# Performance work log

Measured on AMD Instinct MI355X. Metric: run time of the kernel, lower is better.

## Reference

```python
import jax, jax.numpy as jnp
import numpy as np

N_HEAD = 4

def setup_inputs() -> dict:
    key = jax.random.key(0)
    ks = jax.random.split(key, 5)
    B, T, C = 2, 4096, 64
    return {
        "x": jax.random.normal(ks[0], (B, T, C), dtype=jnp.float32),
        "w_attn": jax.random.normal(ks[1], (3 * C, C), dtype=jnp.float32) * 0.02,
        "b_attn": jax.random.normal(ks[2], (3 * C,), dtype=jnp.float32) * 0.02,
        "w_proj": jax.random.normal(ks[3], (C, C), dtype=jnp.float32) * 0.02,
        "b_proj": jax.random.normal(ks[4], (C,), dtype=jnp.float32) * 0.02,
    }

def reference(x, w_attn, b_attn, w_proj, b_proj):
    B, T, C = x.shape
    H = N_HEAD
    Dh = C // H
    # fused QKV projection (torch Linear: x @ W.T + b)
    qkv = x @ w_attn.T + b_attn                      # [B,T,3C]
    q, k, v = jnp.split(qkv, 3, axis=-1)             # each [B,T,C]
    q = q.reshape(B, T, H, Dh).transpose(0, 2, 1, 3)  # [B,H,T,Dh]
    k = k.reshape(B, T, H, Dh).transpose(0, 2, 1, 3)
    v = v.reshape(B, T, H, Dh).transpose(0, 2, 1, 3)
    scale = 1.0 / np.sqrt(Dh).astype(np.float32)
    scores = jnp.einsum("bhqd,bhkd->bhqk", q, k) * scale  # [B,H,T,T]
    attn = jax.nn.softmax(scores, axis=-1)
    y = jnp.einsum("bhqk,bhkd->bhqd", attn, v)       # [B,H,T,Dh]
    y = y.transpose(0, 2, 1, 3).reshape(B, T, C)     # [B,T,C]
    return y @ w_proj.T + b_proj
```

## Files before the change

### kernel.cpp

```cpp
#include <hip/hip_runtime.h>
#include <math.h>

#define BB 2
#define TT 4096
#define CC 64
#define HH 4
#define DH 16
#define NROW (BB*TT)
#define SCALE 0.36067376022224085f

typedef __fp16 h4 __attribute__((ext_vector_type(4)));
typedef __fp16 h2 __attribute__((ext_vector_type(2)));
typedef float  f4 __attribute__((ext_vector_type(4)));

__global__ __launch_bounds__(256) void qkv_kernel(const float* __restrict__ x,
        const float* __restrict__ w, const float* __restrict__ bias,
        __fp16* __restrict__ Q, __fp16* __restrict__ K, __fp16* __restrict__ VT) {
    __shared__ __fp16 smv[64][16];
    const int t = threadIdx.x;
    const int wave = t >> 6, lane = t & 63;
    const int lq = lane & 15, g = lane >> 4;
    const int r0 = blockIdx.x*16;
    const int b = r0 >> 12, tt0 = r0 & (TT-1);

    h4 xb[4];
    const float* xrow = x + (size_t)(r0 + lq)*CC;
    #pragma unroll
    for (int s = 0; s < 4; s++) {
        float4 xv = *(const float4*)(xrow + s*16 + g*4);
        h2 lo = __builtin_amdgcn_cvt_pkrtz(xv.x, xv.y);
        h2 hi = __builtin_amdgcn_cvt_pkrtz(xv.z, xv.w);
        xb[s] = (h4){lo.x, lo.y, hi.x, hi.y};
    }

    #pragma unroll
    for (int j = 0; j < 3; j++) {
        const int nt = wave*3 + j;
        const int o0 = nt*16;
        const float sc = (nt < 4) ? SCALE : 1.0f;
        float4 bv = *(const float4*)(bias + o0 + g*4);
        f4 acc = {bv.x*sc, bv.y*sc, bv.z*sc, bv.w*sc};
        #pragma unroll
        for (int s = 0; s < 4; s++) {
            float4 wv = *(const float4*)(w + (size_t)(o0 + lq)*CC + s*16 + g*4);
            h2 lo = __builtin_amdgcn_cvt_pkrtz(wv.x*sc, wv.y*sc);
            h2 hi = __builtin_amdgcn_cvt_pkrtz(wv.z*sc, wv.w*sc);
            h4 af = (h4){lo.x, lo.y, hi.x, hi.y};
            acc = __builtin_amdgcn_mfma_f32_16x16x16f16(af, xb[s], acc, 0, 0, 0);
        }
        h2 plo = __builtin_amdgcn_cvt_pkrtz(acc.x, acc.y);
        h2 phi = __builtin_amdgcn_cvt_pkrtz(acc.z, acc.w);
        h4 pk = (h4){plo.x, plo.y, phi.x, phi.y};
        if (nt < 8) {
            const int part = nt >> 2, h = nt & 3;
            __fp16* dst = (part == 0) ? Q : K;
            *(h4*)(dst + ((size_t)(b*HH + h)*TT + tt0 + lq)*DH + g*4) = pk;
        } else {
            const int h = nt - 8;
            smv[h*16 + g*4 + 0][lq] = pk.x;
            smv[h*16 + g*4 + 1][lq] = pk.y;
            smv[h*16 + g*4 + 2][lq] = pk.z;
            smv[h*16 + g*4 + 3][lq] = pk.w;
        }
    }
    __syncthreads();
    if (t < 64) {
        const int h = t >> 4, d = t & 15;
        uint4 v0 = *(const uint4*)&smv[t][0];
        uint4 v1 = *(const uint4*)&smv[t][8];
        __fp16* dst = VT + (size_t)(b*HH + h)*TT*DH
                        + (size_t)((tt0 >> 6)*16 + d)*64 + (tt0 & 63);
        *(uint4*)dst = v0;
        *(uint4*)(dst + 8) = v1;
    }
}

__global__ __launch_bounds__(256) void attn_kernel(const __fp16* __restrict__ Q,
        const __fp16* __restrict__ K, const __fp16* __restrict__ VT,
        __fp16* __restrict__ yh) {
    __shared__ f4    Osm[4][4][64];
    __shared__ float Lsm[4][4][64];
    const int t = threadIdx.x;
    const int wave = t >> 6, lane = t & 63;
    const int lq = lane & 15, g = lane >> 4;
    const int head = blockIdx.x >> 6;
    const int qt   = blockIdx.x & 63;
    const int q0 = qt*64;
    const __fp16* Qh = Q  + (size_t)head*TT*DH;
    const __fp16* Kh = K  + (size_t)head*TT*DH;
    const __fp16* Vh = VT + (size_t)head*TT*DH;

    h4 qf[4];
    #pragma unroll
    for (int h = 0; h < 4; h++)
        qf[h] = *(const h4*)(Qh + (size_t)(q0 + h*16 + lq)*DH + g*4);

    f4 O[4];
    float lp[4];
    #pragma unroll
    for (int h = 0; h < 4; h++) { O[h] = (f4){0.f,0.f,0.f,0.f}; lp[h] = 0.f; }

    const __fp16* kbase = Kh + (size_t)(wave*1024 + lq)*DH + g*4;
    const __fp16* vbase = Vh + (size_t)(wave*16)*1024 + lq*64 + g*4;

    const int start = (blockIdx.x*5 + wave*3) & 15;

    h4 ka[4], va[4], kb[4], vb[4];
    {
        const int c0 = start;
        #pragma unroll
        for (int s = 0; s < 4; s++) {
            ka[s] = *(const h4*)(kbase + (size_t)c0*64*DH + (size_t)s*16*DH);
            va[s] = *(const h4*)(vbase + (size_t)c0*1024 + s*16);
        }
    }

#define ATTN_CHUNK(KF, VF)                                                        \
    {                                                                             \
        const f4 z = {0.f, 0.f, 0.f, 0.f};                                        \
        _Pragma("unroll")                                                         \
        for (int h = 0; h < 4; h++) {                                             \
            f4 S0 = __builtin_amdgcn_mfma_f32_16x16x16f16(KF[0], qf[h], z, 0,0,0);\
            f4 S1 = __builtin_amdgcn_mfma_f32_16x16x16f16(KF[1], qf[h], z, 0,0,0);\
            f4 S2 = __builtin_amdgcn_mfma_f32_16x16x16f16(KF[2], qf[h], z, 0,0,0);\
            f4 S3 = __builtin_amdgcn_mfma_f32_16x16x16f16(KF[3], qf[h], z, 0,0,0);\
            float p0, p1, p2, p3; h2 lo, hi; h4 P; float lacc = 0.f;              \
            p0 = __builtin_amdgcn_exp2f(S0.x); p1 = __builtin_amdgcn_exp2f(S0.y); \
            p2 = __builtin_amdgcn_exp2f(S0.z); p3 = __builtin_amdgcn_exp2f(S0.w); \
            lacc += p0 + p1 + p2 + p3;                                            \
            lo = __builtin_amdgcn_cvt_pkrtz(p0, p1);                              \
            hi = __builtin_amdgcn_cvt_pkrtz(p2, p3);                              \
            P = (h4){lo.x, lo.y, hi.x, hi.y};                                     \
            O[h] = __builtin_amdgcn_mfma_f32_16x16x16f16(VF[0], P, O[h], 0,0,0);  \
            p0 = __builtin_amdgcn_exp2f(S1.x); p1 = __builtin_amdgcn_exp2f(S1.y); \
            p2 = __builtin_amdgcn_exp2f(S1.z); p3 = __builtin_amdgcn_exp2f(S1.w); \
            lacc += p0 + p1 + p2 + p3;                                            \
            lo = __builtin_amdgcn_cvt_pkrtz(p0, p1);                              \
            hi = __builtin_amdgcn_cvt_pkrtz(p2, p3);                              \
            P = (h4){lo.x, lo.y, hi.x, hi.y};                                     \
            O[h] = __builtin_amdgcn_mfma_f32_16x16x16f16(VF[1], P, O[h], 0,0,0);  \
            p0 = __builtin_amdgcn_exp2f(S2.x); p1 = __builtin_amdgcn_exp2f(S2.y); \
            p2 = __builtin_amdgcn_exp2f(S2.z); p3 = __builtin_amdgcn_exp2f(S2.w); \
            lacc += p0 + p1 + p2 + p3;                                            \
            lo = __builtin_amdgcn_cvt_pkrtz(p0, p1);                              \
            hi = __builtin_amdgcn_cvt_pkrtz(p2, p3);                              \
            P = (h4){lo.x, lo.y, hi.x, hi.y};                                     \
            O[h] = __builtin_amdgcn_mfma_f32_16x16x16f16(VF[2], P, O[h], 0,0,0);  \
            p0 = __builtin_amdgcn_exp2f(S3.x); p1 = __builtin_amdgcn_exp2f(S3.y); \
            p2 = __builtin_amdgcn_exp2f(S3.z); p3 = __builtin_amdgcn_exp2f(S3.w); \
            lacc += p0 + p1 + p2 + p3;                                            \
            lo = __builtin_amdgcn_cvt_pkrtz(p0, p1);                              \
            hi = __builtin_amdgcn_cvt_pkrtz(p2, p3);                              \
            P = (h4){lo.x, lo.y, hi.x, hi.y};                                     \
            O[h] = __builtin_amdgcn_mfma_f32_16x16x16f16(VF[3], P, O[h], 0,0,0);  \
            lp[h] += lacc;                                                        \
        }                                                                         \
    }

    for (int it = 0; it < 16; it += 2) {
        {
            const int c1 = (start + it + 1) & 15;
            #pragma unroll
            for (int s = 0; s < 4; s++) {
                kb[s] = *(const h4*)(kbase + (size_t)c1*64*DH + (size_t)s*16*DH);
                vb[s] = *(const h4*)(vbase + (size_t)c1*1024 + s*16);
            }
        }
        ATTN_CHUNK(ka, va)
        {
            const int c2 = (start + it + 2) & 15;
            #pragma unroll
            for (int s = 0; s < 4; s++) {
                ka[s] = *(const h4*)(kbase + (size_t)c2*64*DH + (size_t)s*16*DH);
                va[s] = *(const h4*)(vbase + (size_t)c2*1024 + s*16);
            }
        }
        ATTN_CHUNK(kb, vb)
    }
#undef ATTN_CHUNK

    #pragma unroll
    for (int h = 0; h < 4; h++) {
        Osm[wave][h][lane] = O[h];
        Lsm[wave][h][lane] = lp[h];
    }
    __syncthreads();

    f4 Os = Osm[0][wave][lane];
    Os += Osm[1][wave][lane];
    Os += Osm[2][wave][lane];
    Os += Osm[3][wave][lane];
    float L = 0.f;
    #pragma unroll
    for (int ks = 0; ks < 4; ks++)
        #pragma unroll
        for (int gg = 0; gg < 4; gg++)
            L += Lsm[ks][wave][gg*16 + lq];
    const float rinv = 1.f / L;
    h2 lo = __builtin_amdgcn_cvt_pkrtz(Os.x*rinv, Os.y*rinv);
    h2 hi = __builtin_amdgcn_cvt_pkrtz(Os.z*rinv, Os.w*rinv);
    h4 pk = (h4){lo.x, lo.y, hi.x, hi.y};
    const int b = head >> 2, hh = head & 3;
    *(h4*)(yh + ((size_t)b*TT + q0 + wave*16 + lq)*CC + hh*DH + g*4) = pk;
}

__global__ __launch_bounds__(256) void proj_kernel(const __fp16* __restrict__ yh,
        const float* __restrict__ w, const float* __restrict__ bias,
        float* __restrict__ out) {
    const int t = threadIdx.x;
    const int wave = t >> 6, lane = t & 63;
    const int lq = lane & 15, g = lane >> 4;
    const int r0 = blockIdx.x*16;
    const int o0 = wave*16;

    h4 yb[4];
    const __fp16* yrow = yh + (size_t)(r0 + lq)*CC;
    #pragma unroll
    for (int s = 0; s < 4; s++) yb[s] = *(const h4*)(yrow + s*16 + g*4);

    float4 bv = *(const float4*)(bias + o0 + g*4);
    f4 acc = {bv.x, bv.y, bv.z, bv.w};
    #pragma unroll
    for (int s = 0; s < 4; s++) {
        float4 wv = *(const float4*)(w + (size_t)(o0 + lq)*CC + s*16 + g*4);
        h2 lo = __builtin_amdgcn_cvt_pkrtz(wv.x, wv.y);
        h2 hi = __builtin_amdgcn_cvt_pkrtz(wv.z, wv.w);
        h4 af = (h4){lo.x, lo.y, hi.x, hi.y};
        acc = __builtin_amdgcn_mfma_f32_16x16x16f16(af, yb[s], acc, 0, 0, 0);
    }
    *(float4*)(out + (size_t)(r0 + lq)*CC + o0 + g*4) = (float4){acc.x, acc.y, acc.z, acc.w};
}

extern "C" void kernel_launch(void* const* d_in, const int* in_sizes, int n_in,
                              void* d_out, int out_size, void* d_ws, size_t ws_size,
                              hipStream_t stream) {
    const float* x      = (const float*)d_in[0];
    const float* w_attn = (const float*)d_in[1];
    const float* b_attn = (const float*)d_in[2];
    const float* w_proj = (const float*)d_in[3];
    const float* b_proj = (const float*)d_in[4];
    float* out = (float*)d_out;

    const size_t headsz = (size_t)BB*HH*TT*DH;
    __fp16* Q   = (__fp16*)d_ws;
    __fp16* K   = Q + headsz;
    __fp16* VT  = K + headsz;
    __fp16* yh  = VT + headsz;

    qkv_kernel<<<NROW/16, 256, 0, stream>>>(x, w_attn, b_attn, Q, K, VT);
    attn_kernel<<<BB*HH*(TT/64), 256, 0, stream>>>(Q, K, VT, yh);
    proj_kernel<<<NROW/16, 256, 0, stream>>>(yh, w_proj, b_proj, out);
}
```

Measured before the change: 95.05 us.

## Store Q/K/V/y in MFMA-fragment-native layout for 32-byte contiguous loads

Changes the layouts written by the QKV and attention kernels so that each lane's four MFMA operand fragments sit contiguously, 16 halfs per lane per 64-row chunk. The attention and projection kernels can then load them with two 16-byte vector loads instead of four 8-byte gathers. The per-wave rotated chunk start order is removed, so waves now walk the K/V chunks sequentially, and the final prefetch is clamped to stay in bounds. The aim is fewer, wider and fully coalesced memory instructions in the hot loop. The cost is more complex indexing in the producers, and dropping the staggered start may raise cache or bank contention between waves.

```diff
diff --git a/kernel.cpp b/kernel.cpp
--- a/kernel.cpp
+++ b/kernel.cpp
@@ -12,6 +12,15 @@
 typedef __fp16 h4 __attribute__((ext_vector_type(4)));
 typedef __fp16 h2 __attribute__((ext_vector_type(2)));
 typedef float  f4 __attribute__((ext_vector_type(4)));
+
+
+union U32B { struct { uint4 a, b; } u; h4 f[4]; };
+__device__ __forceinline__ U32B ld32(const __fp16* p) {
+    U32B r;
+    r.u.a = *(const uint4*)p;
+    r.u.b = *(const uint4*)(p + 8);
+    return r;
+}
 
 __global__ __launch_bounds__(256) void qkv_kernel(const float* __restrict__ x,
         const float* __restrict__ w, const float* __restrict__ bias,
@@ -22,6 +31,7 @@
     const int lq = lane & 15, g = lane >> 4;
     const int r0 = blockIdx.x*16;
     const int b = r0 >> 12, tt0 = r0 & (TT-1);
+    const int chunk = tt0 >> 6, seg = (tt0 >> 4) & 3;
 
     h4 xb[4];
     const float* xrow = x + (size_t)(r0 + lq)*CC;
@@ -53,8 +63,9 @@
         h4 pk = (h4){plo.x, plo.y, phi.x, phi.y};
         if (nt < 8) {
             const int part = nt >> 2, h = nt & 3;
-            __fp16* dst = (part == 0) ? Q : K;
-            *(h4*)(dst + ((size_t)(b*HH + h)*TT + tt0 + lq)*DH + g*4) = pk;
+            __fp16* dst = ((part == 0) ? Q : K)
+                + (size_t)(b*HH + h)*(TT*DH) + chunk*1024 + lane*16 + seg*4;
+            *(h4*)dst = pk;
         } else {
             const int h = nt - 8;
             smv[h*16 + g*4 + 0][lq] = pk.x;
@@ -64,14 +75,11 @@
         }
     }
     __syncthreads();
-    if (t < 64) {
-        const int h = t >> 4, d = t & 15;
-        uint4 v0 = *(const uint4*)&smv[t][0];
-        uint4 v1 = *(const uint4*)&smv[t][8];
-        __fp16* dst = VT + (size_t)(b*HH + h)*TT*DH
-                        + (size_t)((tt0 >> 6)*16 + d)*64 + (tt0 & 63);
-        *(uint4*)dst = v0;
-        *(uint4*)(dst + 8) = v1;
+    {
+        const int h = t >> 6, n = t & 63;
+        h4 vv = *(const h4*)&smv[h*16 + (n & 15)][(n >> 4)*4];
+        __fp16* dst = VT + (size_t)(b*HH + h)*(TT*DH) + chunk*1024 + n*16 + seg*4;
+        *(h4*)dst = vv;
     }
 }
 
@@ -90,40 +98,28 @@
     const __fp16* Kh = K  + (size_t)head*TT*DH;
     const __fp16* Vh = VT + (size_t)head*TT*DH;
 
-    h4 qf[4];
-    #pragma unroll
-    for (int h = 0; h < 4; h++)
-        qf[h] = *(const h4*)(Qh + (size_t)(q0 + h*16 + lq)*DH + g*4);
+    U32B qfu = ld32(Qh + (size_t)qt*1024 + lane*16);
 
     f4 O[4];
     float lp[4];
     #pragma unroll
     for (int h = 0; h < 4; h++) { O[h] = (f4){0.f,0.f,0.f,0.f}; lp[h] = 0.f; }
 
-    const __fp16* kbase = Kh + (size_t)(wave*1024 + lq)*DH + g*4;
-    const __fp16* vbase = Vh + (size_t)(wave*16)*1024 + lq*64 + g*4;
-
-    const int start = (blockIdx.x*5 + wave*3) & 15;
-
-    h4 ka[4], va[4], kb[4], vb[4];
-    {
-        const int c0 = start;
-        #pragma unroll
-        for (int s = 0; s < 4; s++) {
-            ka[s] = *(const h4*)(kbase + (size_t)c0*64*DH + (size_t)s*16*DH);
-            va[s] = *(const h4*)(vbase + (size_t)c0*1024 + s*16);
-        }
-    }
+    const __fp16* kbase = Kh + (size_t)(wave*16)*1024 + lane*16;
+    const __fp16* vbase = Vh + (size_t)(wave*16)*1024 + lane*16;
+
+    U32B ka = ld32(kbase), va = ld32(vbase);
+    U32B kb, vb;
 
 #define ATTN_CHUNK(KF, VF)                                                        \
     {                                                                             \
         const f4 z = {0.f, 0.f, 0.f, 0.f};                                        \
         _Pragma("unroll")                                                         \
         for (int h = 0; h < 4; h++) {                                             \
-            f4 S0 = __builtin_amdgcn_mfma_f32_16x16x16f16(KF[0], qf[h], z, 0,0,0);\
-            f4 S1 = __builtin_amdgcn_mfma_f32_16x16x16f16(KF[1], qf[h], z, 0,0,0);\
-            f4 S2 = __builtin_amdgcn_mfma_f32_16x16x16f16(KF[2], qf[h], z, 0,0,0);\
-            f4 S3 = __builtin_amdgcn_mfma_f32_16x16x16f16(KF[3], qf[h], z, 0,0,0);\
+            f4 S0 = __builtin_amdgcn_mfma_f32_16x16x16f16(KF.f[0], qfu.f[h], z, 0,0,0);\
+            f4 S1 = __builtin_amdgcn_mfma_f32_16x16x16f16(KF.f[1], qfu.f[h], z, 0,0,0);\
+            f4 S2 = __builtin_amdgcn_mfma_f32_16x16x16f16(KF.f[2], qfu.f[h], z, 0,0,0);\
+            f4 S3 = __builtin_amdgcn_mfma_f32_16x16x16f16(KF.f[3], qfu.f[h], z, 0,0,0);\
             float p0, p1, p2, p3; h2 lo, hi; h4 P; float lacc = 0.f;              \
             p0 = __builtin_amdgcn_exp2f(S0.x); p1 = __builtin_amdgcn_exp2f(S0.y); \
             p2 = __builtin_amdgcn_exp2f(S0.z); p3 = __builtin_amdgcn_exp2f(S0.w); \
@@ -131,49 +127,40 @@
             lo = __builtin_amdgcn_cvt_pkrtz(p0, p1);                              \
             hi = __builtin_amdgcn_cvt_pkrtz(p2, p3);                              \
             P = (h4){lo.x, lo.y, hi.x, hi.y};                                     \
-            O[h] = __builtin_amdgcn_mfma_f32_16x16x16f16(VF[0], P, O[h], 0,0,0);  \
+            O[h] = __builtin_amdgcn_mfma_f32_16x16x16f16(VF.f[0], P, O[h], 0,0,0);\
             p0 = __builtin_amdgcn_exp2f(S1.x); p1 = __builtin_amdgcn_exp2f(S1.y); \
             p2 = __builtin_amdgcn_exp2f(S1.z); p3 = __builtin_amdgcn_exp2f(S1.w); \
             lacc += p0 + p1 + p2 + p3;                                            \
             lo = __builtin_amdgcn_cvt_pkrtz(p0, p1);                              \
             hi = __builtin_amdgcn_cvt_pkrtz(p2, p3);                              \
             P = (h4){lo.x, lo.y, hi.x, hi.y};                                     \
-            O[h] = __builtin_amdgcn_mfma_f32_16x16x16f16(VF[1], P, O[h], 0,0,0);  \
+            O[h] = __builtin_amdgcn_mfma_f32_16x16x16f16(VF.f[1], P, O[h], 0,0,0);\
             p0 = __builtin_amdgcn_exp2f(S2.x); p1 = __builtin_amdgcn_exp2f(S2.y); \
             p2 = __builtin_amdgcn_exp2f(S2.z); p3 = __builtin_amdgcn_exp2f(S2.w); \
             lacc += p0 + p1 + p2 + p3;                                            \
             lo = __builtin_amdgcn_cvt_pkrtz(p0, p1);                              \
             hi = __builtin_amdgcn_cvt_pkrtz(p2, p3);                              \
             P = (h4){lo.x, lo.y, hi.x, hi.y};                                     \
-            O[h] = __builtin_amdgcn_mfma_f32_16x16x16f16(VF[2], P, O[h], 0,0,0);  \
+            O[h] = __builtin_amdgcn_mfma_f32_16x16x16f16(VF.f[2], P, O[h], 0,0,0);\
             p0 = __builtin_amdgcn_exp2f(S3.x); p1 = __builtin_amdgcn_exp2f(S3.y); \
             p2 = __builtin_amdgcn_exp2f(S3.z); p3 = __builtin_amdgcn_exp2f(S3.w); \
             lacc += p0 + p1 + p2 + p3;                                            \
             lo = __builtin_amdgcn_cvt_pkrtz(p0, p1);                              \
             hi = __builtin_amdgcn_cvt_pkrtz(p2, p3);                              \
             P = (h4){lo.x, lo.y, hi.x, hi.y};                                     \
-            O[h] = __builtin_amdgcn_mfma_f32_16x16x16f16(VF[3], P, O[h], 0,0,0);  \
+            O[h] = __builtin_amdgcn_mfma_f32_16x16x16f16(VF.f[3], P, O[h], 0,0,0);\
             lp[h] += lacc;                                                        \
         }                                                                         \
     }
 
     for (int it = 0; it < 16; it += 2) {
-        {
-            const int c1 = (start + it + 1) & 15;
-            #pragma unroll
-            for (int s = 0; s < 4; s++) {
-                kb[s] = *(const h4*)(kbase + (size_t)c1*64*DH + (size_t)s*16*DH);
-                vb[s] = *(const h4*)(vbase + (size_t)c1*1024 + s*16);
-            }
-        }
+        kb = ld32(kbase + (size_t)(it + 1)*1024);
+        vb = ld32(vbase + (size_t)(it + 1)*1024);
         ATTN_CHUNK(ka, va)
         {
-            const int c2 = (start + it + 2) & 15;
-            #pragma unroll
-            for (int s = 0; s < 4; s++) {
-                ka[s] = *(const h4*)(kbase + (size_t)c2*64*DH + (size_t)s*16*DH);
-                va[s] = *(const h4*)(vbase + (size_t)c2*1024 + s*16);
-            }
+            const int c2 = (it + 2 < 16) ? it + 2 : 15;
+            ka = ld32(kbase + (size_t)c2*1024);
+            va = ld32(vbase + (size_t)c2*1024);
         }
         ATTN_CHUNK(kb, vb)
     }
@@ -201,7 +188,8 @@
     h2 hi = __builtin_amdgcn_cvt_pkrtz(Os.z*rinv, Os.w*rinv);
     h4 pk = (h4){lo.x, lo.y, hi.x, hi.y};
     const int b = head >> 2, hh = head & 3;
-    *(h4*)(yh + ((size_t)b*TT + q0 + wave*16 + lq)*CC + hh*DH + g*4) = pk;
+    const size_t rblk = ((size_t)b*TT + q0) / 16 + wave;
+    *(h4*)(yh + rblk*1024 + lane*16 + hh*4) = pk;
 }
 
 __global__ __launch_bounds__(256) void proj_kernel(const __fp16* __restrict__ yh,
@@ -213,10 +201,7 @@
     const int r0 = blockIdx.x*16;
     const int o0 = wave*16;
 
-    h4 yb[4];
-    const __fp16* yrow = yh + (size_t)(r0 + lq)*CC;
-    #pragma unroll
-    for (int s = 0; s < 4; s++) yb[s] = *(const h4*)(yrow + s*16 + g*4);
+    U32B yb = ld32(yh + (size_t)blockIdx.x*1024 + lane*16);
 
     float4 bv = *(const float4*)(bias + o0 + g*4);
     f4 acc = {bv.x, bv.y, bv.z, bv.w};
@@ -226,7 +211,7 @@
         h2 lo = __builtin_amdgcn_cvt_pkrtz(wv.x, wv.y);
         h2 hi = __builtin_amdgcn_cvt_pkrtz(wv.z, wv.w);
         h4 af = (h4){lo.x, lo.y, hi.x, hi.y};
-        acc = __builtin_amdgcn_mfma_f32_16x16x16f16(af, yb[s], acc, 0, 0, 0);
+        acc = __builtin_amdgcn_mfma_f32_16x16x16f16(af, yb.f[s], acc, 0, 0, 0);
     }
     *(float4*)(out + (size_t)(r0 + lq)*CC + o0 + g*4) = (float4){acc.x, acc.y, acc.z, acc.w};
 }
```

New measurement: 96.26 us. About the same (+1.3%).
